# Kernel tuning notes

Measured on AMD Instinct MI355X. Metric: run time of the kernel, lower is better.

The kernel has to match this reference:

```python
import jax, jax.numpy as jnp
import numpy as np
import math

D_MODEL = 1024
NUM_HEADS = 16
B, L = 2, 2048
# scale_level=0, patch_time_span=1 -> effective_stride=1
PERIODS = (1.0, 30.0)
WEIGHTS = (0.8, 0.4)
SIGMAS = (0.5, 2.0)


def setup_inputs() -> dict:
    key = jax.random.key(0)
    ks = jax.random.split(key, 10)
    s = 1.0 / math.sqrt(D_MODEL)
    inp = {
        "x": jax.random.normal(ks[0], (B, L, D_MODEL), dtype=jnp.float32),
        "Wq": jax.random.normal(ks[1], (D_MODEL, D_MODEL), dtype=jnp.float32) * s,
        "bq": jax.random.normal(ks[2], (D_MODEL,), dtype=jnp.float32) * 0.01,
        "Wk": jax.random.normal(ks[3], (D_MODEL, D_MODEL), dtype=jnp.float32) * s,
        "bk": jax.random.normal(ks[4], (D_MODEL,), dtype=jnp.float32) * 0.01,
        "Wv": jax.random.normal(ks[5], (D_MODEL, D_MODEL), dtype=jnp.float32) * s,
        "bv": jax.random.normal(ks[6], (D_MODEL,), dtype=jnp.float32) * 0.01,
        "Wo": jax.random.normal(ks[7], (D_MODEL, D_MODEL), dtype=jnp.float32) * s,
        "bo": jax.random.normal(ks[8], (D_MODEL,), dtype=jnp.float32) * 0.01,
        "prior_lambda": jnp.asarray(2.0, dtype=jnp.float32),
    }
    return inp


def _gaussian_mask(length):
    idx = jnp.arange(length, dtype=jnp.float32)
    delta = jnp.abs(idx[:, None] - idx[None, :])  # [L, L]
    mask = jnp.zeros_like(delta)
    for p, w, sigma in zip(PERIODS, WEIGHTS, SIGMAS):
        if p < 0.2:
            continue
        mask = mask + w * jnp.exp(-((delta - p) ** 2) / (2.0 * sigma ** 2))
    return mask


def reference(x, Wq, bq, Wk, bk, Wv, bv, Wo, bo, prior_lambda):
    Bx, Lx, D = x.shape
    H = NUM_HEADS
    hd = D // H

    def split_heads(t):  # [B, L, D] -> [B, H, L, hd]
        return t.reshape(Bx, Lx, H, hd).transpose(0, 2, 1, 3)

    Q = split_heads(x @ Wq.T + bq)
    K = split_heads(x @ Wk.T + bk)
    V = split_heads(x @ Wv.T + bv)

    scores = jnp.einsum("bhqd,bhkd->bhqk", Q, K) / math.sqrt(hd)
    scores = scores + prior_lambda * _gaussian_mask(Lx)[None, None, :, :]
    attn = jax.nn.softmax(scores, axis=-1)
    out = jnp.einsum("bhqk,bhkd->bhqd", attn, V)
    out = out.transpose(0, 2, 1, 3).reshape(Bx, Lx, D)
    return out @ Wo.T + bo
```

## Files before the change

kernel.cpp:

```cpp
#include <hip/hip_runtime.h>

#define D_MODEL 1024
#define SEQ_L   2048
#define NHEADS  16
#define HDIM    64
#define NROWS   4096

#define QSCALE 0.18033688011112042f
#define LOG2E  1.4426950408889634f

#if __has_builtin(__builtin_amdgcn_exp2f)
#define EXP2F(x) __builtin_amdgcn_exp2f(x)
#else
#define EXP2F(x) __expf((x) * 0.6931471805599453f)
#endif

typedef __attribute__((ext_vector_type(8))) short short8;
typedef __attribute__((ext_vector_type(4))) short short4v;
typedef __attribute__((ext_vector_type(4))) float floatx4;
typedef __attribute__((ext_vector_type(4))) unsigned short ushort4v;
typedef unsigned short ushort;

static __device__ __forceinline__ ushort f2bf(float f) {
    unsigned int u = __float_as_uint(f);
    u += 0x7FFFu + ((u >> 16) & 1u);
    return (ushort)(u >> 16);
}

static __device__ __forceinline__ floatx4 mfma16(short8 a, short8 b, floatx4 c) {
    return __builtin_amdgcn_mfma_f32_16x16x32_bf16(a, b, c, 0, 0, 0);
}

static __device__ __forceinline__ void store8bf(ushort* dst, float4 a, float4 b) {
    uint4 pk;
    pk.x = (unsigned)f2bf(a.x) | ((unsigned)f2bf(a.y) << 16);
    pk.y = (unsigned)f2bf(a.z) | ((unsigned)f2bf(a.w) << 16);
    pk.z = (unsigned)f2bf(b.x) | ((unsigned)f2bf(b.y) << 16);
    pk.w = (unsigned)f2bf(b.z) | ((unsigned)f2bf(b.w) << 16);
    *(uint4*)dst = pk;
}

static __device__ __forceinline__ void gll16(const ushort* g, ushort* l) {
    __builtin_amdgcn_global_load_lds(
        (const __attribute__((address_space(1))) unsigned int*)(const unsigned int*)g,
        (__attribute__((address_space(3))) unsigned int*)(unsigned int*)l,
        16, 0, 0);
}

__global__ __launch_bounds__(256) void convert_bf16(
    const float* __restrict__ x,
    const float* __restrict__ wq, const float* __restrict__ wk,
    const float* __restrict__ wv, const float* __restrict__ wo,
    ushort* __restrict__ xb, ushort* __restrict__ wb3, ushort* __restrict__ wob)
{
    const int seg = blockIdx.y;
    const float* src;
    ushort* dst;
    int n;
    if      (seg == 0) { src = x;  dst = xb;                n = 4194304; }
    else if (seg == 1) { src = wq; dst = wb3;               n = 1048576; }
    else if (seg == 2) { src = wk; dst = wb3 + 1048576;     n = 1048576; }
    else if (seg == 3) { src = wv; dst = wb3 + 2097152;     n = 1048576; }
    else               { src = wo; dst = wob;               n = 1048576; }
    const int i = (blockIdx.x * 256 + threadIdx.x) * 8;
    if (i >= n) return;
    float4 a = *(const float4*)(src + i);
    float4 b = *(const float4*)(src + i + 4);
    store8bf(dst + i, a, b);
}

__global__ __launch_bounds__(256, 4) void gemm_qkv(
    const ushort* __restrict__ A, const ushort* __restrict__ B,
    const float* __restrict__ bq, const float* __restrict__ bk,
    const float* __restrict__ bv,
    ushort* __restrict__ Qo, ushort* __restrict__ Ko, ushort* __restrict__ Vo)
{
    __shared__ ushort As[64 * 64];
    __shared__ ushort Bs[128 * 64];

    const int tid  = threadIdx.x;
    const int w    = tid >> 6;
    const int lane = tid & 63;
    const int l15  = lane & 15;
    const int quad = lane >> 4;

    const int bm = blockIdx.y * 64;
    const int bn = blockIdx.x * 128;
    const int z  = blockIdx.x >> 3;

    const int ciA0 = tid,        ciA1 = tid + 256;
    const int rA0 = ciA0 >> 3,   rA1 = ciA1 >> 3;
    const int sA0i = ciA0 & 7,   sA1i = ciA1 & 7;
    const ushort* aP0 = A + (size_t)(bm + rA0) * 1024 + (sA0i ^ (rA0 & 7)) * 8;
    const ushort* aP1 = A + (size_t)(bm + rA1) * 1024 + (sA1i ^ (rA1 & 7)) * 8;
    ushort* lA0 = &As[rA0 * 64 + sA0i * 8];
    ushort* lA1 = &As[rA1 * 64 + sA1i * 8];

    const ushort* bP[4];
    ushort* lB[4];
#pragma unroll
    for (int p = 0; p < 4; p++) {
        const int ci = tid + p * 256;
        const int r = ci >> 3, s = ci & 7;
        bP[p] = B + (size_t)(bn + r) * 1024 + (s ^ (r & 7)) * 8;
        lB[p] = &Bs[r * 64 + s * 8];
    }

    const int x7 = l15 & 7;

    floatx4 acc[4][2];
#pragma unroll
    for (int i = 0; i < 4; i++)
#pragma unroll
        for (int j = 0; j < 2; j++) acc[i][j] = (floatx4){0.f, 0.f, 0.f, 0.f};

    for (int k0 = 0; k0 < 1024; k0 += 64) {
        __syncthreads();
        gll16(aP0 + k0, lA0);
        gll16(aP1 + k0, lA1);
#pragma unroll
        for (int p = 0; p < 4; p++) gll16(bP[p] + k0, lB[p]);
        __syncthreads();

#pragma unroll
        for (int kk = 0; kk < 2; kk++) {
            const int slot = ((kk * 4 + quad) ^ x7) * 8;
            short8 af[4], bf[2];
#pragma unroll
            for (int mi = 0; mi < 4; mi++)
                af[mi] = *(const short8*)&As[(mi * 16 + l15) * 64 + slot];
#pragma unroll
            for (int ni = 0; ni < 2; ni++)
                bf[ni] = *(const short8*)&Bs[(w * 32 + ni * 16 + l15) * 64 + slot];
            if (z == 2) {
#pragma unroll
                for (int mi = 0; mi < 4; mi++)
#pragma unroll
                    for (int ni = 0; ni < 2; ni++)
                        acc[mi][ni] = mfma16(af[mi], bf[ni], acc[mi][ni]);
            } else {
#pragma unroll
                for (int mi = 0; mi < 4; mi++)
#pragma unroll
                    for (int ni = 0; ni < 2; ni++)
                        acc[mi][ni] = mfma16(bf[ni], af[mi], acc[mi][ni]);
            }
        }
    }

    __syncthreads();
    ushort* St = Bs;
    const int cwbase = bn & 1023;
    const int bb = bm >> 11;

    if (z == 2) {
#pragma unroll
        for (int ni = 0; ni < 2; ni++) {
            const int hdp = w * 32 + ni * 16 + l15;
            const float bvl = bv[cwbase + hdp];
            const int xr = (hdp & 7) << 1;
#pragma unroll
            for (int mi = 0; mi < 4; mi++) {
                ushort4v pk;
#pragma unroll
                for (int r = 0; r < 4; r++) pk[r] = f2bf(acc[mi][ni][r] + bvl);
                const int gs = (mi * 4 + quad) ^ xr;
                *(ushort4v*)&St[hdp * 64 + gs * 4] = pk;
            }
        }
        __syncthreads();
        const int li0 = bm & 2047;
        const int c = lane & 7;
#pragma unroll
        for (int t = 0; t < 4; t++) {
            const int hdp = w * 32 + t * 8 + (lane >> 3);
            const int h  = (cwbase >> 6) + (hdp >> 6);
            const int hd = hdp & 63;
            const int gs = (2 * c) ^ ((hdp & 7) << 1);
            uint4 vdat = *(const uint4*)&St[hdp * 64 + gs * 4];
            *(uint4*)(Vo + ((size_t)(bb * NHEADS + h) * HDIM + hd) * SEQ_L + li0 + c * 8) = vdat;
        }
    } else {
        const float* bias = z ? bk : bq;
        const float scale = z ? 1.0f : QSCALE;
        ushort* outp = z ? Ko : Qo;
#pragma unroll
        for (int ni = 0; ni < 2; ni++) {
            const int colw = cwbase + w * 32 + ni * 16 + quad * 4;
            const float4 bb4 = *(const float4*)&bias[colw];
#pragma unroll
            for (int mi = 0; mi < 4; mi++) {
                const int row = mi * 16 + l15;
                ushort4v pk;
                pk[0] = f2bf((acc[mi][ni][0] + bb4.x) * scale);
                pk[1] = f2bf((acc[mi][ni][1] + bb4.y) * scale);
                pk[2] = f2bf((acc[mi][ni][2] + bb4.z) * scale);
                pk[3] = f2bf((acc[mi][ni][3] + bb4.w) * scale);
                const int gs = (w * 8 + ni * 4 + quad) ^ ((row & 7) << 2);
                *(ushort4v*)&St[row * 128 + gs * 4] = pk;
            }
        }
        __syncthreads();
        const int c = l15;
        const int h0 = cwbase >> 6;
        const int h  = h0 + (c >> 3);
        const int hd0 = (c & 7) * 8;
#pragma unroll
        for (int t = 0; t < 4; t++) {
            const int row = w * 16 + t * 4 + quad;
            const int li = (bm + row) & 2047;
            const int gs = (2 * c) ^ ((row & 7) << 2);
            uint4 vdat = *(const uint4*)&St[row * 128 + gs * 4];
            *(uint4*)(outp + ((size_t)(bb * NHEADS + h) * SEQ_L + li) * HDIM + hd0) = vdat;
        }
    }
}

__global__ __launch_bounds__(256, 4) void attn(
    const ushort* __restrict__ Q,
    const ushort* __restrict__ K,
    const ushort* __restrict__ Vt,
    const float* __restrict__ lam,
    ushort* __restrict__ Aout)
{
    __shared__ float mtab[128];
    __shared__ ushort Ks[2][64 * 64];
    __shared__ ushort Vts[2][64 * 64];

    const int tid  = threadIdx.x;
    const int wave = tid >> 6;
    const int lane = tid & 63;
    const int l15  = lane & 15;
    const int quad = lane >> 4;

    const int qb = blockIdx.x;
    const int h  = blockIdx.y;
    const int bz = blockIdx.z;
    const int bh = bz * NHEADS + h;
    const int q0 = qb * 64;

    const float lambda = *lam;
    if (tid < 128) {
        float d  = (float)tid;
        float e1 = (d - 1.f) * (d - 1.f);
        float e2 = (d - 30.f) * (d - 30.f);
        mtab[tid] = LOG2E * lambda *
                    (0.8f * __expf(-2.0f * e1) + 0.4f * __expf(-0.125f * e2));
    }

    const ushort* qp =
        Q + ((size_t)bh * SEQ_L + q0 + wave * 16 + l15) * HDIM + quad * 8;
    short8 qf[2];
    qf[0] = *(const short8*)qp;
    qf[1] = *(const short8*)(qp + 32);

    const ushort* kbase = K  + ((size_t)bh * SEQ_L) * HDIM;
    const ushort* vbase = Vt + ((size_t)bh * HDIM) * SEQ_L;

    const int cid0 = tid, cid1 = 256 + tid;
    const int row0 = cid0 >> 3, row1 = cid1 >> 3;
    const int cl0  = (cid0 & 7) ^ (row0 & 7);
    const int cl1  = (cid1 & 7) ^ (row1 & 7);
    const ushort* kg0 = kbase + (size_t)row0 * HDIM + cl0 * 8;
    const ushort* kg1 = kbase + (size_t)row1 * HDIM + cl1 * 8;
    const ushort* vg0 = vbase + (size_t)row0 * SEQ_L + cl0 * 8;
    const ushort* vg1 = vbase + (size_t)row1 * SEQ_L + cl1 * 8;

    floatx4 o[4];
#pragma unroll
    for (int i = 0; i < 4; i++) o[i] = (floatx4){0.f, 0.f, 0.f, 0.f};
    floatx4 ol = (floatx4){0.f, 0.f, 0.f, 0.f};

    uint4 onesw;
    onesw.x = 0x3F803F80u; onesw.y = 0x3F803F80u;
    onesw.z = 0x3F803F80u; onesw.w = 0x3F803F80u;
    const short8 ones8 = __builtin_bit_cast(short8, onesw);

    gll16(kg0, &Ks[0][cid0 * 8]);
    gll16(kg1, &Ks[0][cid1 * 8]);
    gll16(vg0, &Vts[0][cid0 * 8]);
    gll16(vg1, &Vts[0][cid1 * 8]);

    const int xo = l15 & 7;

    for (int t = 0; t < 32; t++) {
        const int cur = t & 1;
        __syncthreads();
        if (t + 1 < 32) {
            const int nxt = cur ^ 1;
            const int koff = (t + 1) * 64;
            gll16(kg0 + (size_t)koff * HDIM, &Ks[nxt][cid0 * 8]);
            gll16(kg1 + (size_t)koff * HDIM, &Ks[nxt][cid1 * 8]);
            gll16(vg0 + koff, &Vts[nxt][cid0 * 8]);
            gll16(vg1 + koff, &Vts[nxt][cid1 * 8]);
        }

        floatx4 s[4];
#pragma unroll
        for (int i = 0; i < 4; i++) s[i] = (floatx4){0.f, 0.f, 0.f, 0.f};
#pragma unroll
        for (int kk = 0; kk < 2; kk++) {
#pragma unroll
            for (int nt = 0; nt < 4; nt++) {
                const int slot = (kk * 4 + quad) ^ xo;
                short8 kf = *(const short8*)&Ks[cur][(nt * 16 + l15) * 64 + slot * 8];
                s[nt] = mfma16(kf, qf[kk], s[nt]);
            }
        }

        const int tg = t - qb;
        if (tg >= -1 && tg <= 1) {
            const int qg = q0 + wave * 16 + l15;
#pragma unroll
            for (int nt = 0; nt < 4; nt++) {
                const int kgi = t * 64 + nt * 16 + quad * 4;
#pragma unroll
                for (int r = 0; r < 4; r++) {
                    int dq = qg - (kgi + r);
                    int ad = dq < 0 ? -dq : dq;
                    s[nt][r] += mtab[ad];
                }
            }
        }

        short8 pb8[2];
#pragma unroll
        for (int c = 0; c < 2; c++) {
            unsigned ur[8];
#pragma unroll
            for (int r = 0; r < 4; r++)
                ur[r] = __float_as_uint(EXP2F(s[2 * c][r])) + 0x8000u;
#pragma unroll
            for (int r = 0; r < 4; r++)
                ur[4 + r] = __float_as_uint(EXP2F(s[2 * c + 1][r])) + 0x8000u;
            uint4 pk;
            pk.x = __builtin_amdgcn_perm(ur[1], ur[0], 0x07060302u);
            pk.y = __builtin_amdgcn_perm(ur[3], ur[2], 0x07060302u);
            pk.z = __builtin_amdgcn_perm(ur[5], ur[4], 0x07060302u);
            pk.w = __builtin_amdgcn_perm(ur[7], ur[6], 0x07060302u);
            pb8[c] = __builtin_bit_cast(short8, pk);
        }

#pragma unroll
        for (int c = 0; c < 2; c++) {
#pragma unroll
            for (int nt = 0; nt < 4; nt++) {
                const int glo = ((c << 2) + (quad >> 1)) ^ xo;
                const int ghi = glo ^ 2;
                const int rb  = (nt * 16 + l15) * 64 + (quad & 1) * 4;
                short4v vlo = *(const short4v*)&Vts[cur][rb + glo * 8];
                short4v vhi = *(const short4v*)&Vts[cur][rb + ghi * 8];
                short8 vf8 = __builtin_shufflevector(vlo, vhi, 0, 1, 2, 3, 4, 5, 6, 7);
                o[nt] = mfma16(vf8, pb8[c], o[nt]);
            }
            ol = mfma16(ones8, pb8[c], ol);
        }
    }

    const float linv = 1.0f / ol[0];
    const int qg = q0 + wave * 16 + l15;
    ushort* obase = Aout + ((size_t)bz * SEQ_L + qg) * D_MODEL + h * HDIM;
#pragma unroll
    for (int nt = 0; nt < 4; nt++) {
        ushort4v pk;
#pragma unroll
        for (int r = 0; r < 4; r++) pk[r] = f2bf(o[nt][r] * linv);
        *(ushort4v*)(obase + nt * 16 + quad * 4) = pk;
    }
}

__global__ __launch_bounds__(256, 4) void gemm_out(
    const ushort* __restrict__ A, const ushort* __restrict__ B,
    const float* __restrict__ bo, float* __restrict__ out)
{
    __shared__ ushort As[64 * 64];
    __shared__ ushort Bs[64 * 64];

    const int tid  = threadIdx.x;
    const int w    = tid >> 6;
    const int lane = tid & 63;
    const int l15  = lane & 15;
    const int quad = lane >> 4;

    const int bm = blockIdx.y * 64;
    const int bn = blockIdx.x * 64;

    const int ci0 = tid, ci1 = tid + 256;
    const int r0 = ci0 >> 3, r1 = ci1 >> 3;
    const int s0 = ci0 & 7,  s1 = ci1 & 7;
    const ushort* aP0 = A + (size_t)(bm + r0) * 1024 + (s0 ^ (r0 & 7)) * 8;
    const ushort* aP1 = A + (size_t)(bm + r1) * 1024 + (s1 ^ (r1 & 7)) * 8;
    const ushort* bP0 = B + (size_t)(bn + r0) * 1024 + (s0 ^ (r0 & 7)) * 8;
    const ushort* bP1 = B + (size_t)(bn + r1) * 1024 + (s1 ^ (r1 & 7)) * 8;
    ushort* lA0 = &As[r0 * 64 + s0 * 8];
    ushort* lA1 = &As[r1 * 64 + s1 * 8];
    ushort* lB0 = &Bs[r0 * 64 + s0 * 8];
    ushort* lB1 = &Bs[r1 * 64 + s1 * 8];

    const int x7 = l15 & 7;

    floatx4 acc[4];
#pragma unroll
    for (int i = 0; i < 4; i++) acc[i] = (floatx4){0.f, 0.f, 0.f, 0.f};

    for (int k0 = 0; k0 < 1024; k0 += 64) {
        __syncthreads();
        gll16(aP0 + k0, lA0);
        gll16(aP1 + k0, lA1);
        gll16(bP0 + k0, lB0);
        gll16(bP1 + k0, lB1);
        __syncthreads();

#pragma unroll
        for (int kk = 0; kk < 2; kk++) {
            const int slot = ((kk * 4 + quad) ^ x7) * 8;
            short8 bf = *(const short8*)&Bs[(w * 16 + l15) * 64 + slot];
#pragma unroll
            for (int mi = 0; mi < 4; mi++) {
                short8 af = *(const short8*)&As[(mi * 16 + l15) * 64 + slot];
                acc[mi] = mfma16(bf, af, acc[mi]);
            }
        }
    }

    const int col0 = bn + w * 16 + quad * 4;
    const float4 bb4 = *(const float4*)&bo[col0];
#pragma unroll
    for (int mi = 0; mi < 4; mi++) {
        const int row = bm + mi * 16 + l15;
        float4 st;
        st.x = acc[mi][0] + bb4.x;
        st.y = acc[mi][1] + bb4.y;
        st.z = acc[mi][2] + bb4.z;
        st.w = acc[mi][3] + bb4.w;
        *(float4*)(out + (size_t)row * 1024 + col0) = st;
    }
}

extern "C" void kernel_launch(void* const* d_in, const int* in_sizes, int n_in,
                              void* d_out, int out_size, void* d_ws, size_t ws_size,
                              hipStream_t stream)
{
    const float* x   = (const float*)d_in[0];
    const float* Wq  = (const float*)d_in[1];
    const float* bq  = (const float*)d_in[2];
    const float* Wk  = (const float*)d_in[3];
    const float* bk  = (const float*)d_in[4];
    const float* Wv  = (const float*)d_in[5];
    const float* bv  = (const float*)d_in[6];
    const float* Wo  = (const float*)d_in[7];
    const float* bo  = (const float*)d_in[8];
    const float* lam = (const float*)d_in[9];
    float* out = (float*)d_out;

    const size_t NELEM = (size_t)NROWS * D_MODEL;
    ushort* Qw  = (ushort*)d_ws;
    ushort* Kw  = Qw + NELEM;
    ushort* Vw  = Kw + NELEM;
    ushort* XA  = Vw + NELEM;
    ushort* Wb3 = XA + NELEM;
    ushort* Wob = Wb3 + 3 * 1024 * 1024;

    dim3 gc(2048, 5);
    convert_bf16<<<gc, 256, 0, stream>>>(x, Wq, Wk, Wv, Wo, XA, Wb3, Wob);

    dim3 g1(3072 / 128, NROWS / 64);
    gemm_qkv<<<g1, 256, 0, stream>>>(XA, Wb3, bq, bk, bv, Qw, Kw, Vw);

    dim3 g2(SEQ_L / 64, NHEADS, 2);
    attn<<<g2, 256, 0, stream>>>(Qw, Kw, Vw, lam, XA);

    dim3 g3(1024 / 64, NROWS / 64);
    gemm_out<<<g3, 256, 0, stream>>>(XA, Wob, bo, out);
}
```

Before: 204.2 us.

## Process two 64-row query groups per attention block to reuse K/V tiles

```diff
diff --git a/kernel.cpp b/kernel.cpp
--- a/kernel.cpp
+++ b/kernel.cpp
@@ -237,7 +237,7 @@
     const int h  = blockIdx.y;
     const int bz = blockIdx.z;
     const int bh = bz * NHEADS + h;
-    const int q0 = qb * 64;
+    const int q0 = qb * 128;
 
     const float lambda = *lam;
     if (tid < 128) {
@@ -250,9 +250,11 @@
 
     const ushort* qp =
         Q + ((size_t)bh * SEQ_L + q0 + wave * 16 + l15) * HDIM + quad * 8;
-    short8 qf[2];
-    qf[0] = *(const short8*)qp;
-    qf[1] = *(const short8*)(qp + 32);
+    short8 qf[2][2];
+    qf[0][0] = *(const short8*)qp;
+    qf[0][1] = *(const short8*)(qp + 32);
+    qf[1][0] = *(const short8*)(qp + 64 * HDIM);
+    qf[1][1] = *(const short8*)(qp + 64 * HDIM + 32);
 
     const ushort* kbase = K  + ((size_t)bh * SEQ_L) * HDIM;
     const ushort* vbase = Vt + ((size_t)bh * HDIM) * SEQ_L;
@@ -266,10 +268,14 @@
     const ushort* vg0 = vbase + (size_t)row0 * SEQ_L + cl0 * 8;
     const ushort* vg1 = vbase + (size_t)row1 * SEQ_L + cl1 * 8;
 
-    floatx4 o[4];
-#pragma unroll
-    for (int i = 0; i < 4; i++) o[i] = (floatx4){0.f, 0.f, 0.f, 0.f};
-    floatx4 ol = (floatx4){0.f, 0.f, 0.f, 0.f};
+    floatx4 o[2][4];
+#pragma unroll
+    for (int g = 0; g < 2; g++)
+#pragma unroll
+        for (int i = 0; i < 4; i++) o[g][i] = (floatx4){0.f, 0.f, 0.f, 0.f};
+    floatx4 ol[2];
+    ol[0] = (floatx4){0.f, 0.f, 0.f, 0.f};
+    ol[1] = (floatx4){0.f, 0.f, 0.f, 0.f};
 
     uint4 onesw;
     onesw.x = 0x3F803F80u; onesw.y = 0x3F803F80u;
@@ -295,50 +301,59 @@
             gll16(vg1 + koff, &Vts[nxt][cid1 * 8]);
         }
 
-        floatx4 s[4];
-#pragma unroll
-        for (int i = 0; i < 4; i++) s[i] = (floatx4){0.f, 0.f, 0.f, 0.f};
+        floatx4 s[2][4];
+#pragma unroll
+        for (int g = 0; g < 2; g++)
+#pragma unroll
+            for (int i = 0; i < 4; i++) s[g][i] = (floatx4){0.f, 0.f, 0.f, 0.f};
 #pragma unroll
         for (int kk = 0; kk < 2; kk++) {
 #pragma unroll
             for (int nt = 0; nt < 4; nt++) {
                 const int slot = (kk * 4 + quad) ^ xo;
                 short8 kf = *(const short8*)&Ks[cur][(nt * 16 + l15) * 64 + slot * 8];
-                s[nt] = mfma16(kf, qf[kk], s[nt]);
-            }
-        }
-
-        const int tg = t - qb;
-        if (tg >= -1 && tg <= 1) {
-            const int qg = q0 + wave * 16 + l15;
-#pragma unroll
-            for (int nt = 0; nt < 4; nt++) {
-                const int kgi = t * 64 + nt * 16 + quad * 4;
-#pragma unroll
-                for (int r = 0; r < 4; r++) {
-                    int dq = qg - (kgi + r);
-                    int ad = dq < 0 ? -dq : dq;
-                    s[nt][r] += mtab[ad];
+                s[0][nt] = mfma16(kf, qf[0][kk], s[0][nt]);
+                s[1][nt] = mfma16(kf, qf[1][kk], s[1][nt]);
+            }
+        }
+
+#pragma unroll
+        for (int g = 0; g < 2; g++) {
+            const int tg = t - (qb * 2 + g);
+            if (tg >= -1 && tg <= 1) {
+                const int qg = q0 + g * 64 + wave * 16 + l15;
+#pragma unroll
+                for (int nt = 0; nt < 4; nt++) {
+                    const int kgi = t * 64 + nt * 16 + quad * 4;
+#pragma unroll
+                    for (int r = 0; r < 4; r++) {
+                        int dq = qg - (kgi + r);
+                        int ad = dq < 0 ? -dq : dq;
+                        s[g][nt][r] += mtab[ad];
+                    }
                 }
             }
         }
 
-        short8 pb8[2];
-#pragma unroll
-        for (int c = 0; c < 2; c++) {
-            unsigned ur[8];
-#pragma unroll
-            for (int r = 0; r < 4; r++)
-                ur[r] = __float_as_uint(EXP2F(s[2 * c][r])) + 0x8000u;
-#pragma unroll
-            for (int r = 0; r < 4; r++)
-                ur[4 + r] = __float_as_uint(EXP2F(s[2 * c + 1][r])) + 0x8000u;
-            uint4 pk;
-            pk.x = __builtin_amdgcn_perm(ur[1], ur[0], 0x07060302u);
-            pk.y = __builtin_amdgcn_perm(ur[3], ur[2], 0x07060302u);
-            pk.z = __builtin_amdgcn_perm(ur[5], ur[4], 0x07060302u);
-            pk.w = __builtin_amdgcn_perm(ur[7], ur[6], 0x07060302u);
-            pb8[c] = __builtin_bit_cast(short8, pk);
+        short8 pb8[2][2];
+#pragma unroll
+        for (int g = 0; g < 2; g++) {
+#pragma unroll
+            for (int c = 0; c < 2; c++) {
+                unsigned ur[8];
+#pragma unroll
+                for (int r = 0; r < 4; r++)
+                    ur[r] = __float_as_uint(EXP2F(s[g][2 * c][r])) + 0x8000u;
+#pragma unroll
+                for (int r = 0; r < 4; r++)
+                    ur[4 + r] = __float_as_uint(EXP2F(s[g][2 * c + 1][r])) + 0x8000u;
+                uint4 pk;
+                pk.x = __builtin_amdgcn_perm(ur[1], ur[0], 0x07060302u);
+                pk.y = __builtin_amdgcn_perm(ur[3], ur[2], 0x07060302u);
+                pk.z = __builtin_amdgcn_perm(ur[5], ur[4], 0x07060302u);
+                pk.w = __builtin_amdgcn_perm(ur[7], ur[6], 0x07060302u);
+                pb8[g][c] = __builtin_bit_cast(short8, pk);
+            }
         }
 
 #pragma unroll
@@ -351,21 +366,26 @@
                 short4v vlo = *(const short4v*)&Vts[cur][rb + glo * 8];
                 short4v vhi = *(const short4v*)&Vts[cur][rb + ghi * 8];
                 short8 vf8 = __builtin_shufflevector(vlo, vhi, 0, 1, 2, 3, 4, 5, 6, 7);
-                o[nt] = mfma16(vf8, pb8[c], o[nt]);
-            }
-            ol = mfma16(ones8, pb8[c], ol);
-        }
-    }
-
-    const float linv = 1.0f / ol[0];
-    const int qg = q0 + wave * 16 + l15;
-    ushort* obase = Aout + ((size_t)bz * SEQ_L + qg) * D_MODEL + h * HDIM;
-#pragma unroll
-    for (int nt = 0; nt < 4; nt++) {
-        ushort4v pk;
-#pragma unroll
-        for (int r = 0; r < 4; r++) pk[r] = f2bf(o[nt][r] * linv);
-        *(ushort4v*)(obase + nt * 16 + quad * 4) = pk;
+                o[0][nt] = mfma16(vf8, pb8[0][c], o[0][nt]);
+                o[1][nt] = mfma16(vf8, pb8[1][c], o[1][nt]);
+            }
+            ol[0] = mfma16(ones8, pb8[0][c], ol[0]);
+            ol[1] = mfma16(ones8, pb8[1][c], ol[1]);
+        }
+    }
+
+#pragma unroll
+    for (int g = 0; g < 2; g++) {
+        const float linv = 1.0f / ol[g][0];
+        const int qg = q0 + g * 64 + wave * 16 + l15;
+        ushort* obase = Aout + ((size_t)bz * SEQ_L + qg) * D_MODEL + h * HDIM;
+#pragma unroll
+        for (int nt = 0; nt < 4; nt++) {
+            ushort4v pk;
+#pragma unroll
+            for (int r = 0; r < 4; r++) pk[r] = f2bf(o[g][nt][r] * linv);
+            *(ushort4v*)(obase + nt * 16 + quad * 4) = pk;
+        }
     }
 }
 
@@ -467,7 +487,7 @@
     dim3 g1(3072 / 128, NROWS / 64);
     gemm_qkv<<<g1, 256, 0, stream>>>(XA, Wb3, bq, bk, bv, Qw, Kw, Vw);
 
-    dim3 g2(SEQ_L / 64, NHEADS, 2);
+    dim3 g2(SEQ_L / 128, NHEADS, 2);
     attn<<<g2, 256, 0, stream>>>(Qw, Kw, Vw, lam, XA);
 
     dim3 g3(1024 / 64, NROWS / 64);
```

Measured after the change: 192.4 us. -5.7%, faster.
